# Performance work log

Hardware: AMD Instinct MI355X
Metric: run time of the kernel (lower is better)

## Reference

```python
import jax, jax.numpy as jnp
import numpy as np

NUM_FORMULAS = 256
NUM_CONJ_ARR = [6, 9, 12, 15]
DEPTH_ARR = [2, 4, 6]
TEMPERATURE = 2.0
INPUT_DIM = 512
BATCH = 8192

# --- static DNF structure (mirrors build-time indicator matrices) ---
_group = NUM_FORMULAS // len(NUM_CONJ_ARR)                       # 64 formulas per group
_conj_per_formula = np.repeat(np.array(NUM_CONJ_ARR), _group)     # [F]
_CONJ2FORM = np.repeat(np.arange(NUM_FORMULAS), _conj_per_formula)  # [C] = 2688
TOTAL_CONJ = int(_CONJ2FORM.shape[0])
_depths = np.tile(np.array(DEPTH_ARR), TOTAL_CONJ // len(DEPTH_ARR))  # depth per conjunction
_LIT2CONJ = np.repeat(np.arange(TOTAL_CONJ), _depths)             # [L] = 10752
TOTAL_LIT = int(_LIT2CONJ.shape[0])


def setup_inputs() -> dict:
    key = jax.random.key(0)
    k = jax.random.split(key, 6)
    x = jax.random.normal(k[0], (BATCH, INPUT_DIM), jnp.float32)
    # literals_random_mask: binary feature-subset mask per literal (build-time constant)
    random_mask = (jax.random.uniform(k[1], (INPUT_DIM, TOTAL_LIT)) < 0.5).astype(jnp.float32)
    glorot = jnp.sqrt(2.0 / (INPUT_DIM + TOTAL_LIT))
    # weight is pre-multiplied by the random mask at build time
    weight = jax.random.normal(k[2], (INPUT_DIM, TOTAL_LIT), jnp.float32) * glorot * random_mask
    # learnable_binary_mask: soft binary-threshold output in [0, 1]
    learnable_binary_mask = jax.random.uniform(k[3], (INPUT_DIM, TOTAL_LIT), jnp.float32)
    bias = jnp.zeros((TOTAL_LIT,), jnp.float32)
    mu = jax.random.normal(k[4], (NUM_FORMULAS, INPUT_DIM), jnp.float32)
    sigma = 1.0 + 0.1 * jax.random.uniform(k[5], (NUM_FORMULAS,), jnp.float32)
    return {
        "x": x, "weight": weight, "learnable_binary_mask": learnable_binary_mask,
        "bias": bias, "mu": mu, "sigma": sigma,
        "lit2conj": jnp.asarray(_LIT2CONJ, jnp.int32),
        "conj2form": jnp.asarray(_CONJ2FORM, jnp.int32),
    }


def reference(x, weight, learnable_binary_mask, bias, mu, sigma, lit2conj, conj2form):
    # literal projection: tanh(x @ (W * M) + b)             -> [B, L]
    literals = jnp.tanh(x @ (weight * learnable_binary_mask) + bias)
    # soft AND over literals of each conjunction: tanh(sum - d + 1.5)
    and_bias = jax.ops.segment_sum(jnp.ones((TOTAL_LIT,), literals.dtype), lit2conj,
                                   num_segments=TOTAL_CONJ)
    conj_sum = jax.ops.segment_sum(literals.T, lit2conj, num_segments=TOTAL_CONJ).T  # [B, C]
    conj = jnp.tanh(conj_sum - and_bias + 1.5)
    # soft OR over conjunctions of each formula: tanh(sum + d - 1.5)
    or_bias = jax.ops.segment_sum(jnp.ones((TOTAL_CONJ,), conj.dtype), conj2form,
                                  num_segments=NUM_FORMULAS)
    form_sum = jax.ops.segment_sum(conj.T, conj2form, num_segments=NUM_FORMULAS).T   # [B, F]
    dnnf = jnp.tanh(form_sum + or_bias - 1.5)
    # localization: softmax over formulas of temperature-scaled RBF, via GEMM expansion
    sq = (jnp.sum(x * x, axis=1, keepdims=True) - 2.0 * (x @ mu.T)
          + jnp.sum(mu * mu, axis=1)[None, :])                                       # [B, F]
    loc = jax.nn.softmax(TEMPERATURE * jnp.exp(-0.5 * sq / (sigma * sigma)[None, :]), axis=-1)
    return dnnf * loc
```

## Files before the change

### kernel.cpp

```cpp
#include <hip/hip_runtime.h>


#define BATCH 8192
#define IDIM 512
#define NFORM 256
#define NLIT 10752
#define WT_ROWS 11040

#define BM 128
#define BN 96
#define BK 64
#define LITPAD 104

typedef __bf16 bf16x8 __attribute__((ext_vector_type(8)));
typedef float f32x4 __attribute__((ext_vector_type(4)));
typedef unsigned short u16;
typedef unsigned int u32;

__device__ __forceinline__ u16 f2bf(float f) {
  u32 u = __float_as_uint(f);
  u = (u + 0x7fffu + ((u >> 16) & 1u)) >> 16;
  return (u16)u;
}

__device__ __forceinline__ float fast_tanh(float x) {
  float e = __expf(2.0f * x);
  return 1.0f - 2.0f * __builtin_amdgcn_rcpf(e + 1.0f);
}

__device__ __forceinline__ void async_cp16(const void* g, void* l) {
  __builtin_amdgcn_global_load_lds(
      (const u32 __attribute__((address_space(1)))*)g,
      (u32 __attribute__((address_space(3)))*)l, 16, 0, 0);
}


__global__ __launch_bounds__(256) void prep_x(const float* __restrict__ x,
                                              u16* __restrict__ xb,
                                              float* __restrict__ xsq) {
  int row = blockIdx.x, t = threadIdx.x;
  const float2 v = ((const float2*)(x + (size_t)row * IDIM))[t];
  u32 packed = (u32)f2bf(v.x) | ((u32)f2bf(v.y) << 16);
  ((u32*)(xb + (size_t)row * IDIM))[t] = packed;
  __shared__ float red[256];
  red[t] = v.x * v.x + v.y * v.y;
  __syncthreads();
  for (int s = 128; s > 0; s >>= 1) {
    if (t < s) red[t] += red[t + s];
    __syncthreads();
  }
  if (t == 0) xsq[row] = red[0];
}

__global__ __launch_bounds__(256) void prep_w(const float* __restrict__ W,
                                              const float* __restrict__ M,
                                              u16* __restrict__ wt) {
  __shared__ float tile[32][33];
  int l0 = blockIdx.x * 32, k0 = blockIdx.y * 32;
  int tx = threadIdx.x, ty = threadIdx.y;
#pragma unroll
  for (int i = 0; i < 4; ++i) {
    int kk = ty + i * 8;
    size_t g = (size_t)(k0 + kk) * NLIT + l0 + tx;
    tile[kk][tx] = W[g] * M[g];
  }
  __syncthreads();
#pragma unroll
  for (int i = 0; i < 4; ++i) {
    int ll = ty + i * 8;
    wt[(size_t)(l0 + ll) * IDIM + k0 + tx] = f2bf(tile[tx][ll]);
  }
}

__global__ __launch_bounds__(256) void prep_mu(const float* __restrict__ mu,
                                               u16* __restrict__ wt,
                                               float* __restrict__ musq) {
  int b = blockIdx.x, t = threadIdx.x;
  if (b < 256) {
    float s = 0.f;
#pragma unroll
    for (int j = t; j < IDIM; j += 256) {
      float v = mu[(size_t)b * IDIM + j];
      wt[(size_t)(NLIT + b) * IDIM + j] = f2bf(v);
      s += v * v;
    }
    __shared__ float red[256];
    red[t] = s;
    __syncthreads();
    for (int sh = 128; sh > 0; sh >>= 1) {
      if (t < sh) red[t] += red[t + sh];
      __syncthreads();
    }
    if (t == 0) musq[b] = red[0];
  } else {
    int row = NLIT + 256 + (b - 256);
    for (int j = t; j < IDIM; j += 256) wt[(size_t)row * IDIM + j] = 0;
  }
}


__global__ __launch_bounds__(256, 2) void dnnf_gemm(
    const u16* __restrict__ xb, const u16* __restrict__ wt,
    const float* __restrict__ bias, float* __restrict__ form_sum,
    float* __restrict__ dotbuf) {
  __shared__ __align__(16) char smraw[BM * LITPAD * 4];
  u16* sA = (u16*)smraw;
  u16* sB = sA + BM * BK;
  float* slit = (float*)smraw;

  const int tid = threadIdx.x;
  const int wave = tid >> 6, lane = tid & 63;
  const int m0 = blockIdx.y * BM;
  const int n0 = blockIdx.x * BN;
  const int q = lane >> 4, cn = lane & 15;

  f32x4 acc[2][6];
#pragma unroll
  for (int a = 0; a < 2; ++a)
#pragma unroll
    for (int b = 0; b < 6; ++b) acc[a][b] = (f32x4){0.f, 0.f, 0.f, 0.f};

  for (int kt = 0; kt < IDIM; kt += BK) {
#pragma unroll
    for (int i = 0; i < 4; ++i) {
      int c = tid + i * 256;
      int r = c >> 3, kgp = c & 7;
      int kg = kgp ^ (r & 7);
      async_cp16(xb + (size_t)(m0 + r) * IDIM + kt + kg * 8, (char*)sA + c * 16);
    }
#pragma unroll
    for (int i = 0; i < 3; ++i) {
      int c = tid + i * 256;
      int r = c >> 3, kgp = c & 7;
      int kg = kgp ^ (r & 7);
      async_cp16(wt + (size_t)(n0 + r) * IDIM + kt + kg * 8, (char*)sB + c * 16);
    }
    __syncthreads();

#pragma unroll
    for (int ks = 0; ks < 2; ++ks) {
      bf16x8 af[2], bfr[6];
#pragma unroll
      for (int mf = 0; mf < 2; ++mf) {
        int row = wave * 32 + mf * 16 + cn;
        int kg = (ks * 4 + q) ^ (row & 7);
        af[mf] = *(const bf16x8*)((const char*)sA + row * (BK * 2) + kg * 16);
      }
#pragma unroll
      for (int nf = 0; nf < 6; ++nf) {
        int row = nf * 16 + cn;
        int kg = (ks * 4 + q) ^ (row & 7);
        bfr[nf] = *(const bf16x8*)((const char*)sB + row * (BK * 2) + kg * 16);
      }
#pragma unroll
      for (int mf = 0; mf < 2; ++mf)
#pragma unroll
        for (int nf = 0; nf < 6; ++nf)
          acc[mf][nf] = __builtin_amdgcn_mfma_f32_16x16x32_bf16(
              af[mf], bfr[nf], acc[mf][nf], 0, 0, 0);
    }
    __syncthreads();
  }

  if (n0 < NLIT) {
#pragma unroll
    for (int nf = 0; nf < 6; ++nf) {
      int col = nf * 16 + cn;
      float bv = bias[n0 + col];
#pragma unroll
      for (int mf = 0; mf < 2; ++mf)
#pragma unroll
        for (int reg = 0; reg < 4; ++reg) {
          int row = wave * 32 + mf * 16 + q * 4 + reg;
          slit[row * LITPAD + col] = fast_tanh(acc[mf][nf][reg] + bv);
        }
    }
    __syncthreads();

    int r = tid >> 1, half = tid & 1;
    const float* lrow = slit + r * LITPAD + half * 48;
    int c0 = ((n0 + half * 48) / 12) * 3;
    size_t grow = (size_t)(m0 + r) * NFORM;
    float run = 0.f;
    int fprev = -1;
#pragma unroll
    for (int tr = 0; tr < 4; ++tr) {
      const float* p = lrow + tr * 12;
      float s2 = p[0] + p[1];
      float s4 = p[2] + p[3] + p[4] + p[5];
      float s6 = p[6] + p[7] + p[8] + p[9] + p[10] + p[11];
      float v = fast_tanh(s2 - 0.5f) + fast_tanh(s4 - 2.5f) +
                fast_tanh(s6 - 4.5f);
      int c = c0 + tr * 3;
      int f = (c < 384)    ? (c / 6)
              : (c < 960)  ? 64 + (c - 384) / 9
              : (c < 1728) ? 128 + (c - 960) / 12
                           : 192 + (c - 1728) / 15;
      if (f != fprev) {
        if (fprev >= 0) atomicAdd(form_sum + grow + fprev, run);
        fprev = f;
        run = 0.f;
      }
      run += v;
    }
    atomicAdd(form_sum + grow + fprev, run);
  } else {
#pragma unroll
    for (int nf = 0; nf < 6; ++nf) {
      int col = n0 - NLIT + nf * 16 + cn;
      if (col < NFORM) {
#pragma unroll
        for (int mf = 0; mf < 2; ++mf)
#pragma unroll
          for (int reg = 0; reg < 4; ++reg) {
            int row = wave * 32 + mf * 16 + q * 4 + reg;
            dotbuf[(size_t)(m0 + row) * NFORM + col] = acc[mf][nf][reg];
          }
      }
    }
  }
}


__global__ __launch_bounds__(256) void finale(
    const float* __restrict__ form_sum, const float* __restrict__ dotbuf,
    const float* __restrict__ xsq, const float* __restrict__ musq,
    const float* __restrict__ sigma, float* __restrict__ out) {
  int r = blockIdx.x, f = threadIdx.x;
  size_t idx = (size_t)r * NFORM + f;
  float dv = dotbuf[idx];
  float sq = xsq[r] - 2.0f * dv + musq[f];
  float sg = sigma[f];
  float p = __expf(-0.5f * sq / (sg * sg));
  float e = __expf(2.0f * p);
  __shared__ float red[256];
  red[f] = e;
  __syncthreads();
  for (int s = 128; s > 0; s >>= 1) {
    if (f < s) red[f] += red[f + s];
    __syncthreads();
  }
  float denom = red[0];
  float dn = fast_tanh(form_sum[idx] + (float)(6 + 3 * (f >> 6)) - 1.5f);
  out[idx] = dn * (e / denom);
}


extern "C" void kernel_launch(void* const* d_in, const int* in_sizes, int n_in,
                              void* d_out, int out_size, void* d_ws,
                              size_t ws_size, hipStream_t stream) {
  const float* x = (const float*)d_in[0];
  const float* W = (const float*)d_in[1];
  const float* M = (const float*)d_in[2];
  const float* bias = (const float*)d_in[3];
  const float* mu = (const float*)d_in[4];
  const float* sigma = (const float*)d_in[5];
  float* out = (float*)d_out;

  float* form_sum = (float*)d_ws;
  float* dotbuf = form_sum + (size_t)BATCH * NFORM;
  u16* xb = (u16*)(dotbuf + (size_t)BATCH * NFORM);
  u16* wt = xb + (size_t)BATCH * IDIM;
  float* xsq = (float*)(wt + (size_t)WT_ROWS * IDIM);
  float* musq = xsq + BATCH;

  hipMemsetAsync(form_sum, 0, (size_t)BATCH * NFORM * sizeof(float), stream);
  prep_x<<<BATCH, 256, 0, stream>>>(x, xb, xsq);
  prep_w<<<dim3(NLIT / 32, IDIM / 32), dim3(32, 8), 0, stream>>>(W, M, wt);
  prep_mu<<<288, 256, 0, stream>>>(mu, wt, musq);
  dnnf_gemm<<<dim3(WT_ROWS / BN, BATCH / BM), 256, 0, stream>>>(xb, wt, bias,
                                                                form_sum, dotbuf);
  finale<<<BATCH, 256, 0, stream>>>(form_sum, dotbuf, xsq, musq, sigma, out);
}
```

Baseline: 289.6 us.

## Double GEMM M-tile to 256, precompute LDS offsets, and use wave-per-row prep/finale

```diff
diff --git a/kernel.cpp b/kernel.cpp
--- a/kernel.cpp
+++ b/kernel.cpp
@@ -7,10 +7,10 @@
 #define NLIT 10752
 #define WT_ROWS 11040
 
-#define BM 128
+#define BM 256
 #define BN 96
 #define BK 64
-#define LITPAD 104
+#define LITPAD 97
 
 typedef __bf16 bf16x8 __attribute__((ext_vector_type(8)));
 typedef float f32x4 __attribute__((ext_vector_type(4)));
@@ -38,18 +38,21 @@
 __global__ __launch_bounds__(256) void prep_x(const float* __restrict__ x,
                                               u16* __restrict__ xb,
                                               float* __restrict__ xsq) {
-  int row = blockIdx.x, t = threadIdx.x;
-  const float2 v = ((const float2*)(x + (size_t)row * IDIM))[t];
-  u32 packed = (u32)f2bf(v.x) | ((u32)f2bf(v.y) << 16);
-  ((u32*)(xb + (size_t)row * IDIM))[t] = packed;
-  __shared__ float red[256];
-  red[t] = v.x * v.x + v.y * v.y;
-  __syncthreads();
-  for (int s = 128; s > 0; s >>= 1) {
-    if (t < s) red[t] += red[t + s];
-    __syncthreads();
-  }
-  if (t == 0) xsq[row] = red[0];
+  int wave = threadIdx.x >> 6, lane = threadIdx.x & 63;
+  int row = blockIdx.x * 4 + wave;
+  const float4* px = (const float4*)(x + (size_t)row * IDIM);
+  float4 a = px[lane * 2], b = px[lane * 2 + 1];
+  uint4 pk;
+  pk.x = (u32)f2bf(a.x) | ((u32)f2bf(a.y) << 16);
+  pk.y = (u32)f2bf(a.z) | ((u32)f2bf(a.w) << 16);
+  pk.z = (u32)f2bf(b.x) | ((u32)f2bf(b.y) << 16);
+  pk.w = (u32)f2bf(b.z) | ((u32)f2bf(b.w) << 16);
+  ((uint4*)(xb + (size_t)row * IDIM))[lane] = pk;
+  float s = a.x * a.x + a.y * a.y + a.z * a.z + a.w * a.w +
+            b.x * b.x + b.y * b.y + b.z * b.z + b.w * b.w;
+#pragma unroll
+  for (int o = 32; o > 0; o >>= 1) s += __shfl_down(s, o);
+  if (lane == 0) xsq[row] = s;
 }
 
 __global__ __launch_bounds__(256) void prep_w(const float* __restrict__ W,
@@ -99,13 +102,11 @@
 }
 
 
-__global__ __launch_bounds__(256, 2) void dnnf_gemm(
+__global__ __launch_bounds__(256, 3) void dnnf_gemm(
     const u16* __restrict__ xb, const u16* __restrict__ wt,
     const float* __restrict__ bias, float* __restrict__ form_sum,
     float* __restrict__ dotbuf) {
-  __shared__ __align__(16) char smraw[BM * LITPAD * 4];
-  u16* sA = (u16*)smraw;
-  u16* sB = sA + BM * BK;
+  __shared__ __align__(16) char smraw[128 * LITPAD * 4];
   float* slit = (float*)smraw;
 
   const int tid = threadIdx.x;
@@ -114,46 +115,50 @@
   const int n0 = blockIdx.x * BN;
   const int q = lane >> 4, cn = lane & 15;
 
-  f32x4 acc[2][6];
-#pragma unroll
-  for (int a = 0; a < 2; ++a)
+  const int kg8 = (((tid & 7) ^ ((tid >> 3) & 7))) * 8;
+  const u16* pa = xb + (size_t)(m0 + (tid >> 3)) * IDIM + kg8;
+  const u16* pb = wt + (size_t)(n0 + (tid >> 3)) * IDIM + kg8;
+  char* dstA = smraw + tid * 16;
+  char* dstB = smraw + 32768 + tid * 16;
+
+  const int kg0_16 = ((q ^ (cn & 7)) << 4);
+  int offA[4], offB[6];
+#pragma unroll
+  for (int mf = 0; mf < 4; ++mf)
+    offA[mf] = (wave * 64 + mf * 16 + cn) * (BK * 2) + kg0_16;
+#pragma unroll
+  for (int nf = 0; nf < 6; ++nf)
+    offB[nf] = 32768 + (nf * 16 + cn) * (BK * 2) + kg0_16;
+
+  f32x4 acc[4][6];
+#pragma unroll
+  for (int a = 0; a < 4; ++a)
 #pragma unroll
     for (int b = 0; b < 6; ++b) acc[a][b] = (f32x4){0.f, 0.f, 0.f, 0.f};
 
   for (int kt = 0; kt < IDIM; kt += BK) {
 #pragma unroll
-    for (int i = 0; i < 4; ++i) {
-      int c = tid + i * 256;
-      int r = c >> 3, kgp = c & 7;
-      int kg = kgp ^ (r & 7);
-      async_cp16(xb + (size_t)(m0 + r) * IDIM + kt + kg * 8, (char*)sA + c * 16);
-    }
-#pragma unroll
-    for (int i = 0; i < 3; ++i) {
-      int c = tid + i * 256;
-      int r = c >> 3, kgp = c & 7;
-      int kg = kgp ^ (r & 7);
-      async_cp16(wt + (size_t)(n0 + r) * IDIM + kt + kg * 8, (char*)sB + c * 16);
-    }
+    for (int i = 0; i < 8; ++i)
+      async_cp16(pa + (size_t)i * 32 * IDIM, dstA + i * 4096);
+#pragma unroll
+    for (int i = 0; i < 3; ++i)
+      async_cp16(pb + (size_t)i * 32 * IDIM, dstB + i * 4096);
+    pa += BK;
+    pb += BK;
     __syncthreads();
 
 #pragma unroll
     for (int ks = 0; ks < 2; ++ks) {
-      bf16x8 af[2], bfr[6];
-#pragma unroll
-      for (int mf = 0; mf < 2; ++mf) {
-        int row = wave * 32 + mf * 16 + cn;
-        int kg = (ks * 4 + q) ^ (row & 7);
-        af[mf] = *(const bf16x8*)((const char*)sA + row * (BK * 2) + kg * 16);
-      }
-#pragma unroll
-      for (int nf = 0; nf < 6; ++nf) {
-        int row = nf * 16 + cn;
-        int kg = (ks * 4 + q) ^ (row & 7);
-        bfr[nf] = *(const bf16x8*)((const char*)sB + row * (BK * 2) + kg * 16);
-      }
-#pragma unroll
-      for (int mf = 0; mf < 2; ++mf)
+      const int x64 = ks ? 64 : 0;
+      bf16x8 af[4], bfr[6];
+#pragma unroll
+      for (int mf = 0; mf < 4; ++mf)
+        af[mf] = *(const bf16x8*)(smraw + (offA[mf] ^ x64));
+#pragma unroll
+      for (int nf = 0; nf < 6; ++nf)
+        bfr[nf] = *(const bf16x8*)(smraw + (offB[nf] ^ x64));
+#pragma unroll
+      for (int mf = 0; mf < 4; ++mf)
 #pragma unroll
         for (int nf = 0; nf < 6; ++nf)
           acc[mf][nf] = __builtin_amdgcn_mfma_f32_16x16x32_bf16(
@@ -163,57 +168,66 @@
   }
 
   if (n0 < NLIT) {
-#pragma unroll
-    for (int nf = 0; nf < 6; ++nf) {
-      int col = nf * 16 + cn;
-      float bv = bias[n0 + col];
-#pragma unroll
-      for (int mf = 0; mf < 2; ++mf)
-#pragma unroll
-        for (int reg = 0; reg < 4; ++reg) {
-          int row = wave * 32 + mf * 16 + q * 4 + reg;
-          slit[row * LITPAD + col] = fast_tanh(acc[mf][nf][reg] + bv);
+    float bv[6];
+#pragma unroll
+    for (int nf = 0; nf < 6; ++nf) bv[nf] = bias[n0 + nf * 16 + cn];
+
+#pragma unroll
+    for (int ph = 0; ph < 2; ++ph) {
+      if (ph) __syncthreads();
+      if ((wave >> 1) == ph) {
+#pragma unroll
+        for (int nf = 0; nf < 6; ++nf) {
+          int col = nf * 16 + cn;
+#pragma unroll
+          for (int mf = 0; mf < 4; ++mf)
+#pragma unroll
+            for (int reg = 0; reg < 4; ++reg) {
+              int lr = (wave & 1) * 64 + mf * 16 + q * 4 + reg;
+              slit[lr * LITPAD + col] = fast_tanh(acc[mf][nf][reg] + bv[nf]);
+            }
         }
-    }
-    __syncthreads();
-
-    int r = tid >> 1, half = tid & 1;
-    const float* lrow = slit + r * LITPAD + half * 48;
-    int c0 = ((n0 + half * 48) / 12) * 3;
-    size_t grow = (size_t)(m0 + r) * NFORM;
-    float run = 0.f;
-    int fprev = -1;
-#pragma unroll
-    for (int tr = 0; tr < 4; ++tr) {
-      const float* p = lrow + tr * 12;
-      float s2 = p[0] + p[1];
-      float s4 = p[2] + p[3] + p[4] + p[5];
-      float s6 = p[6] + p[7] + p[8] + p[9] + p[10] + p[11];
-      float v = fast_tanh(s2 - 0.5f) + fast_tanh(s4 - 2.5f) +
-                fast_tanh(s6 - 4.5f);
-      int c = c0 + tr * 3;
-      int f = (c < 384)    ? (c / 6)
-              : (c < 960)  ? 64 + (c - 384) / 9
-              : (c < 1728) ? 128 + (c - 960) / 12
-                           : 192 + (c - 1728) / 15;
-      if (f != fprev) {
-        if (fprev >= 0) atomicAdd(form_sum + grow + fprev, run);
-        fprev = f;
-        run = 0.f;
       }
-      run += v;
-    }
-    atomicAdd(form_sum + grow + fprev, run);
+      __syncthreads();
+
+      int r = tid >> 1, half = tid & 1;
+      const float* lrow = slit + r * LITPAD + half * 48;
+      int c0 = ((n0 + half * 48) / 12) * 3;
+      size_t grow = (size_t)(m0 + ph * 128 + r) * NFORM;
+      float run = 0.f;
+      int fprev = -1;
+#pragma unroll
+      for (int tr = 0; tr < 4; ++tr) {
+        const float* p = lrow + tr * 12;
+        float s2 = p[0] + p[1];
+        float s4 = p[2] + p[3] + p[4] + p[5];
+        float s6 = p[6] + p[7] + p[8] + p[9] + p[10] + p[11];
+        float v = fast_tanh(s2 - 0.5f) + fast_tanh(s4 - 2.5f) +
+                  fast_tanh(s6 - 4.5f);
+        int c = c0 + tr * 3;
+        int f = (c < 384)    ? (c / 6)
+                : (c < 960)  ? 64 + (c - 384) / 9
+                : (c < 1728) ? 128 + (c - 960) / 12
+                             : 192 + (c - 1728) / 15;
+        if (f != fprev) {
+          if (fprev >= 0) atomicAdd(form_sum + grow + fprev, run);
+          fprev = f;
+          run = 0.f;
+        }
+        run += v;
+      }
+      atomicAdd(form_sum + grow + fprev, run);
+    }
   } else {
 #pragma unroll
     for (int nf = 0; nf < 6; ++nf) {
       int col = n0 - NLIT + nf * 16 + cn;
       if (col < NFORM) {
 #pragma unroll
-        for (int mf = 0; mf < 2; ++mf)
+        for (int mf = 0; mf < 4; ++mf)
 #pragma unroll
           for (int reg = 0; reg < 4; ++reg) {
-            int row = wave * 32 + mf * 16 + q * 4 + reg;
+            int row = wave * 64 + mf * 16 + q * 4 + reg;
             dotbuf[(size_t)(m0 + row) * NFORM + col] = acc[mf][nf][reg];
           }
       }
@@ -226,23 +240,29 @@
     const float* __restrict__ form_sum, const float* __restrict__ dotbuf,
     const float* __restrict__ xsq, const float* __restrict__ musq,
     const float* __restrict__ sigma, float* __restrict__ out) {
-  int r = blockIdx.x, f = threadIdx.x;
-  size_t idx = (size_t)r * NFORM + f;
-  float dv = dotbuf[idx];
-  float sq = xsq[r] - 2.0f * dv + musq[f];
-  float sg = sigma[f];
-  float p = __expf(-0.5f * sq / (sg * sg));
-  float e = __expf(2.0f * p);
-  __shared__ float red[256];
-  red[f] = e;
-  __syncthreads();
-  for (int s = 128; s > 0; s >>= 1) {
-    if (f < s) red[f] += red[f + s];
-    __syncthreads();
-  }
-  float denom = red[0];
-  float dn = fast_tanh(form_sum[idx] + (float)(6 + 3 * (f >> 6)) - 1.5f);
-  out[idx] = dn * (e / denom);
+  int wave = threadIdx.x >> 6, lane = threadIdx.x & 63;
+  int r = blockIdx.x * 4 + wave;
+  size_t base = (size_t)r * NFORM;
+  float xs = xsq[r];
+  float e[4], s = 0.f;
+#pragma unroll
+  for (int j = 0; j < 4; ++j) {
+    int f = j * 64 + lane;
+    float sq = xs - 2.0f * dotbuf[base + f] + musq[f];
+    float sg = sigma[f];
+    float p = __expf(-0.5f * sq / (sg * sg));
+    e[j] = __expf(2.0f * p);
+    s += e[j];
+  }
+#pragma unroll
+  for (int o = 32; o > 0; o >>= 1) s += __shfl_xor(s, o);
+  float inv = __builtin_amdgcn_rcpf(s);
+#pragma unroll
+  for (int j = 0; j < 4; ++j) {
+    int f = j * 64 + lane;
+    float dn = fast_tanh(form_sum[base + f] + (float)(6 + 3 * j) - 1.5f);
+    out[base + f] = dn * e[j] * inv;
+  }
 }
 
 
@@ -265,10 +285,10 @@
   float* musq = xsq + BATCH;
 
   hipMemsetAsync(form_sum, 0, (size_t)BATCH * NFORM * sizeof(float), stream);
-  prep_x<<<BATCH, 256, 0, stream>>>(x, xb, xsq);
+  prep_x<<<BATCH / 4, 256, 0, stream>>>(x, xb, xsq);
   prep_w<<<dim3(NLIT / 32, IDIM / 32), dim3(32, 8), 0, stream>>>(W, M, wt);
   prep_mu<<<288, 256, 0, stream>>>(mu, wt, musq);
   dnnf_gemm<<<dim3(WT_ROWS / BN, BATCH / BM), 256, 0, stream>>>(xb, wt, bias,
                                                                 form_sum, dotbuf);
-  finale<<<BATCH, 256, 0, stream>>>(form_sum, dotbuf, xsq, musq, sigma, out);
-}
+  finale<<<BATCH / 4, 256, 0, stream>>>(form_sum, dotbuf, xsq, musq, sigma, out);
+}
```

After: 266.3 us. 1.09x faster.
